# Performance work log

Hardware: AMD Instinct MI355X
Metric: run time of the kernel (lower is better)

## Reference

```python
import jax, jax.numpy as jnp
import numpy as np

HEADS = 8
DIM_HEAD = 64
QLEVEL = 127.0  # symmetric int8: clamp to [-128, 127]


def fake_quant(x):
    """Symmetric per-tensor int8 fake quantization with straight-through estimator."""
    delta = jnp.max(jnp.abs(x)) / QLEVEL
    xq = jnp.clip(jnp.round(x / delta), -128.0, 127.0) * delta
    return x + jax.lax.stop_gradient(xq - x)


def setup_inputs() -> dict:
    key = jax.random.key(0)
    ks = jax.random.split(key, 7)
    b, n, m, d, dc = 2, 4096, 1024, 512, 768
    return {
        "x": jax.random.normal(ks[0], (b, n, d), jnp.float32),
        "context": jax.random.normal(ks[1], (b, m, dc), jnp.float32),
        "Wq": jax.random.normal(ks[2], (d, d), jnp.float32) * 0.02,
        "Wk": jax.random.normal(ks[3], (dc, d), jnp.float32) * 0.02,
        "Wv": jax.random.normal(ks[4], (dc, d), jnp.float32) * 0.02,
        "Wo": jax.random.normal(ks[5], (d, d), jnp.float32) * 0.02,
        "bo": jnp.zeros((d,), jnp.float32),
    }


def reference(x, context, Wq, Wk, Wv, Wo, bo):
    b, n, _ = x.shape
    h, dh = HEADS, DIM_HEAD
    scale = dh ** -0.5

    q = x @ Wq            # [b, n, h*dh]
    k = context @ Wk      # [b, m, h*dh]
    v = context @ Wv      # [b, m, h*dh]

    def split(t):  # b n (h d) -> b h n d
        return t.reshape(t.shape[0], t.shape[1], h, dh).transpose(0, 2, 1, 3)

    q, k, v = split(q), split(k), split(v)

    # fake-quantize q and k before the score matmul (use_aq=True path)
    q = fake_quant(q)
    k = fake_quant(k)
    sim = jnp.einsum('bhid,bhjd->bhij', q, k) * scale  # [b, h, n, m]
    attn = jax.nn.softmax(sim, axis=-1)

    # fake-quantize attention weights and v before the AV matmul
    out = jnp.einsum('bhij,bhjd->bhid', fake_quant(attn), fake_quant(v))
    out = out.transpose(0, 2, 1, 3).reshape(b, n, h * dh)  # b h n d -> b n (h d)
    return out @ Wo + bo  # to_out[0]; to_out[-1] is Dropout (identity in eval)
```

## Files before the change

kernel.cpp:

```cpp
#include <hip/hip_runtime.h>
#include <stdint.h>

typedef float  v4f  __attribute__((ext_vector_type(4)));
typedef int    v4i  __attribute__((ext_vector_type(4)));
typedef __bf16 v8bf __attribute__((ext_vector_type(8)));
typedef __bf16 v4bf __attribute__((ext_vector_type(4)));

#define BATCH  2
#define NQ     4096
#define MK     1024
#define DMODEL 512
#define DCTX   768
#define NH     8
#define DH     64

__global__ __launch_bounds__(256) void k_prep(
    const float* __restrict__ x, const float* __restrict__ ctx,
    __bf16* __restrict__ xb, __bf16* __restrict__ cb,
    const float* __restrict__ Wq, const float* __restrict__ Wk,
    const float* __restrict__ Wv, const float* __restrict__ Wo,
    __bf16* __restrict__ Wq_t, __bf16* __restrict__ Wk_t,
    __bf16* __restrict__ Wv_t, __bf16* __restrict__ Wo_t,
    unsigned* __restrict__ scal) {
  int bx = blockIdx.x;
  if (bx < 2816) {
    const int XC = BATCH * NQ * DMODEL / 8;
    const int CC = BATCH * MK * DCTX / 8;
    int idx = bx * 256 + threadIdx.x;
    const float* src; __bf16* dst;
    if (idx < XC) { src = x + (size_t)idx * 8; dst = xb + (size_t)idx * 8; }
    else {
      int j = idx - XC;
      if (j >= CC) return;
      src = ctx + (size_t)j * 8; dst = cb + (size_t)j * 8;
    }
    float4 a = *(const float4*)src, b = *(const float4*)(src + 4);
    v8bf o = { (__bf16)a.x, (__bf16)a.y, (__bf16)a.z, (__bf16)a.w,
               (__bf16)b.x, (__bf16)b.y, (__bf16)b.z, (__bf16)b.w };
    *(v8bf*)dst = o;
    return;
  }
  int id = bx - 2816;
  if (id == 0 && threadIdx.x < 4) scal[threadIdx.x] = 0u;
  int tx = id & 15, rem = id >> 4;
  int ty = rem % 24, tz = rem / 24;
  const float* src; __bf16* dst; int K;
  switch (tz) {
    case 0:  src = Wq; dst = Wq_t; K = DMODEL; break;
    case 1:  src = Wk; dst = Wk_t; K = DCTX;   break;
    case 2:  src = Wv; dst = Wv_t; K = DCTX;   break;
    default: src = Wo; dst = Wo_t; K = DMODEL; break;
  }
  int k0 = ty * 32;
  if (k0 >= K) return;
  int n0 = tx * 32;
  __shared__ __bf16 tile[32][33];
  int c = threadIdx.x & 31, r0 = threadIdx.x >> 5;
  for (int i = 0; i < 4; ++i) {
    int r = r0 + i * 8;
    tile[c][r] = (__bf16)src[(size_t)(k0 + r) * DMODEL + n0 + c];
  }
  __syncthreads();
  for (int i = 0; i < 4; ++i) {
    int r = r0 + i * 8;
    dst[(size_t)(n0 + r) * K + k0 + c] = tile[r][c];
  }
}

template<int K_, int NC, bool BIAS, bool AMAX>
__device__ __forceinline__ void gemm_body(
    char* smemraw, const __bf16* __restrict__ A, const __bf16* __restrict__ Bt,
    float* __restrict__ C, int N, int rowBlk, int colBlk,
    const float* __restrict__ bias,
    unsigned* __restrict__ amaxLo, unsigned* __restrict__ amaxHi) {
  constexpr int CS = K_ + 8;
  constexpr int GPC = K_ / 8;
  constexpr int JT = NC / 16;
  __bf16* Bs = (__bf16*)smemraw;
  float* redmax = (float*)(smemraw + (size_t)NC * CS * 2);
  const int tid = threadIdx.x;
  const int lane = tid & 63, wave = tid >> 6;
  const int l15 = lane & 15, g = lane >> 4;
  const int col0 = colBlk * NC;
  const int row0w = rowBlk * 128 + wave * 32;

#pragma unroll
  for (int i = 0; i < NC * GPC / 256; ++i) {
    int f = i * 256 + tid;
    int c = f / GPC, w = f - c * GPC;
    *(v8bf*)(&Bs[c * CS + w * 8]) =
        *(const v8bf*)(Bt + (size_t)(col0 + c) * K_ + w * 8);
  }
  __syncthreads();

  v4f acc[2][JT] = {};
  const __bf16* a0 = A + (size_t)(row0w + l15) * K_ + g * 8;
  const __bf16* a1 = A + (size_t)(row0w + 16 + l15) * K_ + g * 8;
#pragma unroll
  for (int k0 = 0; k0 < K_; k0 += 32) {
    v8bf af0 = *(const v8bf*)(a0 + k0);
    v8bf af1 = *(const v8bf*)(a1 + k0);
#pragma unroll
    for (int j = 0; j < JT; ++j) {
      v8bf bfj = *(const v8bf*)(&Bs[(j * 16 + l15) * CS + k0 + g * 8]);
      acc[0][j] = __builtin_amdgcn_mfma_f32_16x16x32_bf16(af0, bfj, acc[0][j], 0, 0, 0);
      acc[1][j] = __builtin_amdgcn_mfma_f32_16x16x32_bf16(af1, bfj, acc[1][j], 0, 0, 0);
    }
  }

  float lmax = 0.0f;
#pragma unroll
  for (int j = 0; j < JT; ++j) {
    int col = col0 + j * 16 + l15;
    float bv = BIAS ? bias[col] : 0.0f;
#pragma unroll
    for (int i = 0; i < 2; ++i) {
#pragma unroll
      for (int r = 0; r < 4; ++r) {
        int row = row0w + i * 16 + g * 4 + r;
        float cv = acc[i][j][r] + bv;
        C[(size_t)row * N + col] = cv;
        if (AMAX) lmax = fmaxf(lmax, fabsf(cv));
      }
    }
  }
  if (AMAX) {
    for (int off = 32; off > 0; off >>= 1)
      lmax = fmaxf(lmax, __shfl_xor(lmax, off, 64));
    if (lane == 0) redmax[wave] = lmax;
    __syncthreads();
    if (tid == 0) {
      float bm = fmaxf(fmaxf(redmax[0], redmax[1]), fmaxf(redmax[2], redmax[3]));
      atomicMax(col0 < 512 ? amaxLo : amaxHi, __float_as_uint(bm));
    }
  }
}

__global__ __launch_bounds__(256, 2) void k_gemm_qkv(
    const __bf16* __restrict__ xb, const __bf16* __restrict__ Wq_t,
    float* __restrict__ qf,
    const __bf16* __restrict__ cb, const __bf16* __restrict__ Wkv_t,
    float* __restrict__ kvf, unsigned* __restrict__ scal) {
  __shared__ __align__(16) char smem[64 * (512 + 8) * 2 + 16];
  int bid = blockIdx.x;
  if (bid < 512) {
    gemm_body<512, 64, false, true>(smem, xb, Wq_t, qf, 512,
                                    bid >> 3, bid & 7, nullptr, scal + 0, scal + 0);
  } else {
    int id = bid - 512;
    gemm_body<768, 32, false, true>(smem, cb, Wkv_t, kvf, 1024,
                                    id >> 5, id & 31, nullptr, scal + 1, scal + 2);
  }
}

__global__ __launch_bounds__(256, 2) void k_gemm_out(
    const __bf16* __restrict__ o, const __bf16* __restrict__ Wo_t,
    float* __restrict__ out, const float* __restrict__ bo) {
  __shared__ __align__(16) char smem[64 * (512 + 8) * 2 + 16];
  gemm_body<512, 64, true, false>(smem, o, Wo_t, out, 512,
                                  blockIdx.x >> 3, blockIdx.x & 7, bo,
                                  nullptr, nullptr);
}

__global__ __launch_bounds__(256) void k_quant_kv(
    const float* __restrict__ kvf,
    int8_t* __restrict__ k8, int8_t* __restrict__ v8t,
    const unsigned* __restrict__ scal) {
  __shared__ int8_t tile[64][80];
  int bx = blockIdx.x;
  if (bx < 1024) {
    int j = bx * 256 + threadIdx.x;
    int r = j >> 7;
    int c4 = (j & 127) << 2;
    float4 v = *(const float4*)(kvf + (size_t)r * 1024 + c4);
    float s = 127.0f / __uint_as_float(scal[1]);
    int a0 = __float2int_rn(v.x * s), a1 = __float2int_rn(v.y * s);
    int a2 = __float2int_rn(v.z * s), a3 = __float2int_rn(v.w * s);
    a0 = max(-128, min(127, a0)); a1 = max(-128, min(127, a1));
    a2 = max(-128, min(127, a2)); a3 = max(-128, min(127, a3));
    unsigned p = (unsigned)(a0 & 255) | ((unsigned)(a1 & 255) << 8) |
                 ((unsigned)(a2 & 255) << 16) | ((unsigned)(a3 & 255) << 24);
    *(unsigned*)(k8 + (size_t)j * 4) = p;
    return;
  }
  int id = bx - 1024;
  int bh = id >> 4, b = bh >> 3, h = bh & 7;
  int j0 = (id & 15) * 64;
  const float s = 127.0f / __uint_as_float(scal[2]);
  int t = threadIdx.x;
  int j = t >> 2, dh0 = (t & 3) << 4;
  const float* src = kvf + (size_t)(b * MK + j0 + j) * 1024 + 512 + h * DH + dh0;
#pragma unroll
  for (int i = 0; i < 16; i += 4) {
    float4 v = *(const float4*)(src + i);
    int a0 = __float2int_rn(v.x * s), a1 = __float2int_rn(v.y * s);
    int a2 = __float2int_rn(v.z * s), a3 = __float2int_rn(v.w * s);
    tile[dh0 + i + 0][j] = (int8_t)max(-128, min(127, a0));
    tile[dh0 + i + 1][j] = (int8_t)max(-128, min(127, a1));
    tile[dh0 + i + 2][j] = (int8_t)max(-128, min(127, a2));
    tile[dh0 + i + 3][j] = (int8_t)max(-128, min(127, a3));
  }
  __syncthreads();
  int dh = t >> 2, jb = (t & 3) << 4;
  v4i val = *(const v4i*)(&tile[dh][jb]);
  *(v4i*)(v8t + (size_t)(bh * DH + dh) * MK + j0 + jb) = val;
}

__device__ __forceinline__ v4i quant_pack16(const float* p, float s) {
  v4i out;
#pragma unroll
  for (int q = 0; q < 4; ++q) {
    float4 v = *(const float4*)(p + q * 4);
    int a0 = __float2int_rn(v.x * s), a1 = __float2int_rn(v.y * s);
    int a2 = __float2int_rn(v.z * s), a3 = __float2int_rn(v.w * s);
    a0 = max(-128, min(127, a0)); a1 = max(-128, min(127, a1));
    a2 = max(-128, min(127, a2)); a3 = max(-128, min(127, a3));
    out[q] = (int)((unsigned)(a0 & 255) | ((unsigned)(a1 & 255) << 8) |
                   ((unsigned)(a2 & 255) << 16) | ((unsigned)(a3 & 255) << 24));
  }
  return out;
}

__global__ __launch_bounds__(256, 4) void k_pass1(
    const float* __restrict__ qf, int8_t* __restrict__ q8,
    const int8_t* __restrict__ k8,
    float* __restrict__ invz, unsigned* __restrict__ scal) {
  __shared__ __align__(16) int8_t kbuf[128 * 72];
  __shared__ float mared[4];
  int bh = blockIdx.y, b = bh >> 3, h = bh & 7;
  int wave = threadIdx.x >> 6, lane = threadIdx.x & 63;
  int l15 = lane & 15, g = lane >> 4;
  int row0 = blockIdx.x * 64;
  int myrow = row0 + wave * 16 + l15;
  const float aq = __uint_as_float(scal[0]), ak = __uint_as_float(scal[1]);
  const float alpha2 = (aq * ak) * (0.125f / (127.0f * 127.0f)) * 1.44269504f;
  const float sq = 127.0f / aq;
  const v4i z4 = {0, 0, 0, 0};
  size_t qoff = (size_t)(b * NQ + myrow) * DMODEL + h * DH + g * 16;
  v4i qfrag = quant_pack16(qf + qoff, sq);
  *(v4i*)(q8 + qoff) = qfrag;
  const int8_t* kbase = k8 + (size_t)b * MK * DMODEL + h * DH;
  const int rs = threadIdx.x >> 2, qs = (threadIdx.x & 3) * 16;

  float z[4] = {0.f, 0.f, 0.f, 0.f};
  int mi = -(1 << 30);
  for (int tile = 0; tile < 8; ++tile) {
    __syncthreads();
    *(v4i*)(&kbuf[rs * 72 + qs]) =
        *(const v4i*)(kbase + (size_t)(tile * 128 + rs) * DMODEL + qs);
    *(v4i*)(&kbuf[(rs + 64) * 72 + qs]) =
        *(const v4i*)(kbase + (size_t)(tile * 128 + rs + 64) * DMODEL + qs);
    __syncthreads();
    float zt = z[tile >> 1];
#pragma unroll
    for (int t = 0; t < 8; ++t) {
      v4i kfrag = *(const v4i*)(&kbuf[(t * 16 + l15) * 72 + g * 16]);
      v4i sa = __builtin_amdgcn_mfma_i32_16x16x64_i8(kfrag, qfrag, z4, 0, 0, 0);
      mi = max(mi, max(max(sa[0], sa[1]), max(sa[2], sa[3])));
      float e0 = __builtin_amdgcn_exp2f((float)sa[0] * alpha2);
      float e1 = __builtin_amdgcn_exp2f((float)sa[1] * alpha2);
      float e2 = __builtin_amdgcn_exp2f((float)sa[2] * alpha2);
      float e3 = __builtin_amdgcn_exp2f((float)sa[3] * alpha2);
      zt += (e0 + e1) + (e2 + e3);
    }
    z[tile >> 1] = zt;
  }
#pragma unroll
  for (int i = 0; i < 4; ++i) {
    z[i] += __shfl_xor(z[i], 16, 64);
    z[i] += __shfl_xor(z[i], 32, 64);
  }
  mi = max(mi, __shfl_xor(mi, 16, 64));
  mi = max(mi, __shfl_xor(mi, 32, 64));
  float zt = (z[0] + z[1]) + (z[2] + z[3]);
  float iz = 1.0f / zt;
  if (g == 0) invz[(size_t)bh * NQ + myrow] = iz;
  float ma = __builtin_amdgcn_exp2f((float)mi * alpha2) * iz;
#pragma unroll
  for (int off = 1; off < 16; off <<= 1)
    ma = fmaxf(ma, __shfl_xor(ma, off, 64));
  if (lane == 0) mared[wave] = ma;
  __syncthreads();
  if (threadIdx.x == 0)
    atomicMax(scal + 3,
              __float_as_uint(fmaxf(fmaxf(mared[0], mared[1]),
                                    fmaxf(mared[2], mared[3]))));
}

__global__ __launch_bounds__(256, 4) void k_pass2(
    const int8_t* __restrict__ q8, const int8_t* __restrict__ k8,
    const int8_t* __restrict__ v8t, const float* __restrict__ invz,
    const unsigned* __restrict__ scal, __bf16* __restrict__ o) {
  __shared__ __align__(16) int8_t kbuf[128 * 72];
  __shared__ __align__(16) int8_t vbuf[64 * 152];
  __shared__ __align__(16) int8_t albuf[4][16 * 152];
  int bh = blockIdx.y, b = bh >> 3, h = bh & 7;
  int wave = threadIdx.x >> 6, lane = threadIdx.x & 63;
  int l15 = lane & 15, g = lane >> 4;
  int row0 = blockIdx.x * 64;
  int myrow = row0 + wave * 16 + l15;
  const float aq = __uint_as_float(scal[0]), ak = __uint_as_float(scal[1]);
  const float avv = __uint_as_float(scal[2]), izm = __uint_as_float(scal[3]);
  const float alpha2 = (aq * ak) * (0.125f / (127.0f * 127.0f)) * 1.44269504f;
  const float oscale = (izm / 127.0f) * (avv / 127.0f);
  const float MAGIC = 12582912.0f;
  const v4i z4 = {0, 0, 0, 0};

  v4i qfrag = *(const v4i*)(q8 + (size_t)(b * NQ + myrow) * DMODEL + h * DH + g * 16);
  const float lcr = __builtin_amdgcn_logf(invz[(size_t)bh * NQ + myrow] * (127.0f / izm));
  const int8_t* kbase = k8 + (size_t)b * MK * DMODEL + h * DH;
  const int8_t* vbase = v8t + (size_t)bh * DH * MK;
  int8_t* alds = albuf[wave];
  const int rs = threadIdx.x >> 2, qs = (threadIdx.x & 3) * 16;
  const int vr = threadIdx.x >> 3, vq = (threadIdx.x & 7) * 16;

  v4i pacc[4] = {};
  for (int tile = 0; tile < 8; ++tile) {
    __syncthreads();
    *(v4i*)(&kbuf[rs * 72 + qs]) =
        *(const v4i*)(kbase + (size_t)(tile * 128 + rs) * DMODEL + qs);
    *(v4i*)(&kbuf[(rs + 64) * 72 + qs]) =
        *(const v4i*)(kbase + (size_t)(tile * 128 + rs + 64) * DMODEL + qs);
    *(v4i*)(&vbuf[vr * 152 + vq]) =
        *(const v4i*)(vbase + (size_t)vr * MK + tile * 128 + vq);
    *(v4i*)(&vbuf[(vr + 32) * 152 + vq]) =
        *(const v4i*)(vbase + (size_t)(vr + 32) * MK + tile * 128 + vq);
    __syncthreads();
#pragma unroll
    for (int t = 0; t < 8; ++t) {
      v4i kfrag = *(const v4i*)(&kbuf[(t * 16 + l15) * 72 + g * 16]);
      v4i sa = __builtin_amdgcn_mfma_i32_16x16x64_i8(kfrag, qfrag, z4, 0, 0, 0);
      float f0 = __builtin_amdgcn_exp2f(fmaf((float)sa[0], alpha2, lcr)) + MAGIC;
      float f1 = __builtin_amdgcn_exp2f(fmaf((float)sa[1], alpha2, lcr)) + MAGIC;
      float f2 = __builtin_amdgcn_exp2f(fmaf((float)sa[2], alpha2, lcr)) + MAGIC;
      float f3 = __builtin_amdgcn_exp2f(fmaf((float)sa[3], alpha2, lcr)) + MAGIC;
      unsigned packed = (__float_as_uint(f0) & 255u) |
                        ((__float_as_uint(f1) & 255u) << 8) |
                        ((__float_as_uint(f2) & 255u) << 16) |
                        (__float_as_uint(f3) << 24);
      *(unsigned*)(alds + l15 * 152 + t * 16 + g * 4) = packed;
    }
#pragma unroll
    for (int c = 0; c < 2; ++c) {
      v4i afrag = *(const v4i*)(alds + l15 * 152 + c * 64 + g * 16);
#pragma unroll
      for (int d = 0; d < 4; ++d) {
        v4i bfrag = *(const v4i*)(&vbuf[(d * 16 + l15) * 152 + c * 64 + g * 16]);
        pacc[d] = __builtin_amdgcn_mfma_i32_16x16x64_i8(afrag, bfrag, pacc[d], 0, 0, 0);
      }
    }
  }
  __bf16* obase = o + (size_t)(b * NQ + row0 + wave * 16) * DMODEL + h * DH;
#pragma unroll
  for (int d = 0; d < 4; ++d)
#pragma unroll
    for (int r = 0; r < 4; ++r)
      obase[(size_t)(g * 4 + r) * DMODEL + d * 16 + l15] =
          (__bf16)((float)pacc[d][r] * oscale);
}

extern "C" void kernel_launch(void* const* d_in, const int* in_sizes, int n_in,
                              void* d_out, int out_size, void* d_ws, size_t ws_size,
                              hipStream_t stream) {
  (void)in_sizes; (void)n_in; (void)out_size; (void)ws_size;
  const float* x   = (const float*)d_in[0];
  const float* ctx = (const float*)d_in[1];
  const float* Wq  = (const float*)d_in[2];
  const float* Wk  = (const float*)d_in[3];
  const float* Wv  = (const float*)d_in[4];
  const float* Wo  = (const float*)d_in[5];
  const float* bo  = (const float*)d_in[6];
  float* out = (float*)d_out;

  char* ws = (char*)d_ws;
  size_t off = 0;
  auto alloc = [&](size_t bytes) {
    char* p = ws + off;
    off += (bytes + 255) & ~(size_t)255;
    return p;
  };
  unsigned* scal = (unsigned*)alloc(16);
  __bf16* Wq_t = (__bf16*)alloc((size_t)512 * 512 * 2);
  __bf16* Wk_t = (__bf16*)alloc((size_t)512 * 768 * 2);
  __bf16* Wv_t = (__bf16*)alloc((size_t)512 * 768 * 2);
  __bf16* Wo_t = (__bf16*)alloc((size_t)512 * 512 * 2);
  __bf16* xb   = (__bf16*)alloc((size_t)BATCH * NQ * DMODEL * 2);
  __bf16* cb   = (__bf16*)alloc((size_t)BATCH * MK * DCTX * 2);
  float* qf  = (float*)alloc((size_t)BATCH * NQ * DMODEL * 4);
  float* kvf = (float*)alloc((size_t)BATCH * MK * 1024 * 4);
  int8_t* q8 = (int8_t*)alloc((size_t)BATCH * NQ * DMODEL);
  int8_t* k8 = (int8_t*)alloc((size_t)BATCH * MK * DMODEL);
  int8_t* v8t = (int8_t*)alloc((size_t)BATCH * NH * DH * MK);
  float* invz = (float*)alloc((size_t)BATCH * NH * NQ * 4);
  __bf16* o = (__bf16*)qf;

  k_prep<<<4352, 256, 0, stream>>>(x, ctx, xb, cb, Wq, Wk, Wv, Wo,
                                   Wq_t, Wk_t, Wv_t, Wo_t, scal);
  k_gemm_qkv<<<1024, 256, 0, stream>>>(xb, Wq_t, qf, cb, Wk_t, kvf, scal);
  k_quant_kv<<<1280, 256, 0, stream>>>(kvf, k8, v8t, scal);
  k_pass1<<<dim3(64, 16), 256, 0, stream>>>(qf, q8, k8, invz, scal);
  k_pass2<<<dim3(64, 16), 256, 0, stream>>>(q8, k8, v8t, invz, scal, o);
  k_gemm_out<<<512, 256, 0, stream>>>(o, Wo_t, out, bo);
}
```

Before: 183.3 us.

## Fuse fp32-to-bf16 input conversion into QKV GEMM and prefetch K/V tiles

Drops the separate x/context bf16 conversion pass and converts fp32 activations to bf16 inside the QKV GEMM A-operand load. This removes a full write and reread of the converted inputs. The attention passes now prefetch the next K/V tile into registers while computing on the current one. Pass2 also swaps the MFMA operand order so each lane writes four contiguous bf16 outputs as one vector store. In exchange, the GEMM reads twice as many bytes per A load and keeps more registers live for the prefetch.

```diff
diff --git a/kernel.cpp b/kernel.cpp
--- a/kernel.cpp
+++ b/kernel.cpp
@@ -15,32 +15,12 @@
 #define DH     64
 
 __global__ __launch_bounds__(256) void k_prep(
-    const float* __restrict__ x, const float* __restrict__ ctx,
-    __bf16* __restrict__ xb, __bf16* __restrict__ cb,
     const float* __restrict__ Wq, const float* __restrict__ Wk,
     const float* __restrict__ Wv, const float* __restrict__ Wo,
     __bf16* __restrict__ Wq_t, __bf16* __restrict__ Wk_t,
     __bf16* __restrict__ Wv_t, __bf16* __restrict__ Wo_t,
     unsigned* __restrict__ scal) {
-  int bx = blockIdx.x;
-  if (bx < 2816) {
-    const int XC = BATCH * NQ * DMODEL / 8;
-    const int CC = BATCH * MK * DCTX / 8;
-    int idx = bx * 256 + threadIdx.x;
-    const float* src; __bf16* dst;
-    if (idx < XC) { src = x + (size_t)idx * 8; dst = xb + (size_t)idx * 8; }
-    else {
-      int j = idx - XC;
-      if (j >= CC) return;
-      src = ctx + (size_t)j * 8; dst = cb + (size_t)j * 8;
-    }
-    float4 a = *(const float4*)src, b = *(const float4*)(src + 4);
-    v8bf o = { (__bf16)a.x, (__bf16)a.y, (__bf16)a.z, (__bf16)a.w,
-               (__bf16)b.x, (__bf16)b.y, (__bf16)b.z, (__bf16)b.w };
-    *(v8bf*)dst = o;
-    return;
-  }
-  int id = bx - 2816;
+  int id = blockIdx.x;
   if (id == 0 && threadIdx.x < 4) scal[threadIdx.x] = 0u;
   int tx = id & 15, rem = id >> 4;
   int ty = rem % 24, tz = rem / 24;
@@ -67,9 +47,19 @@
   }
 }
 
-template<int K_, int NC, bool BIAS, bool AMAX>
+__device__ __forceinline__ v8bf load_a8(const __bf16* p) {
+  return *(const v8bf*)p;
+}
+__device__ __forceinline__ v8bf load_a8(const float* p) {
+  float4 a = *(const float4*)p, b = *(const float4*)(p + 4);
+  v8bf o = { (__bf16)a.x, (__bf16)a.y, (__bf16)a.z, (__bf16)a.w,
+             (__bf16)b.x, (__bf16)b.y, (__bf16)b.z, (__bf16)b.w };
+  return o;
+}
+
+template<int K_, int NC, bool BIAS, bool AMAX, typename AT>
 __device__ __forceinline__ void gemm_body(
-    char* smemraw, const __bf16* __restrict__ A, const __bf16* __restrict__ Bt,
+    char* smemraw, const AT* __restrict__ A, const __bf16* __restrict__ Bt,
     float* __restrict__ C, int N, int rowBlk, int colBlk,
     const float* __restrict__ bias,
     unsigned* __restrict__ amaxLo, unsigned* __restrict__ amaxHi) {
@@ -94,12 +84,12 @@
   __syncthreads();
 
   v4f acc[2][JT] = {};
-  const __bf16* a0 = A + (size_t)(row0w + l15) * K_ + g * 8;
-  const __bf16* a1 = A + (size_t)(row0w + 16 + l15) * K_ + g * 8;
+  const AT* a0 = A + (size_t)(row0w + l15) * K_ + g * 8;
+  const AT* a1 = A + (size_t)(row0w + 16 + l15) * K_ + g * 8;
 #pragma unroll
   for (int k0 = 0; k0 < K_; k0 += 32) {
-    v8bf af0 = *(const v8bf*)(a0 + k0);
-    v8bf af1 = *(const v8bf*)(a1 + k0);
+    v8bf af0 = load_a8(a0 + k0);
+    v8bf af1 = load_a8(a1 + k0);
 #pragma unroll
     for (int j = 0; j < JT; ++j) {
       v8bf bfj = *(const v8bf*)(&Bs[(j * 16 + l15) * CS + k0 + g * 8]);
@@ -137,19 +127,21 @@
 }
 
 __global__ __launch_bounds__(256, 2) void k_gemm_qkv(
-    const __bf16* __restrict__ xb, const __bf16* __restrict__ Wq_t,
+    const float* __restrict__ x, const __bf16* __restrict__ Wq_t,
     float* __restrict__ qf,
-    const __bf16* __restrict__ cb, const __bf16* __restrict__ Wkv_t,
+    const float* __restrict__ ctx, const __bf16* __restrict__ Wkv_t,
     float* __restrict__ kvf, unsigned* __restrict__ scal) {
   __shared__ __align__(16) char smem[64 * (512 + 8) * 2 + 16];
   int bid = blockIdx.x;
   if (bid < 512) {
-    gemm_body<512, 64, false, true>(smem, xb, Wq_t, qf, 512,
-                                    bid >> 3, bid & 7, nullptr, scal + 0, scal + 0);
+    gemm_body<512, 64, false, true, float>(smem, x, Wq_t, qf, 512,
+                                           bid >> 3, bid & 7, nullptr,
+                                           scal + 0, scal + 0);
   } else {
     int id = bid - 512;
-    gemm_body<768, 32, false, true>(smem, cb, Wkv_t, kvf, 1024,
-                                    id >> 5, id & 31, nullptr, scal + 1, scal + 2);
+    gemm_body<768, 32, false, true, float>(smem, ctx, Wkv_t, kvf, 1024,
+                                           id >> 5, id & 31, nullptr,
+                                           scal + 1, scal + 2);
   }
 }
 
@@ -157,9 +149,9 @@
     const __bf16* __restrict__ o, const __bf16* __restrict__ Wo_t,
     float* __restrict__ out, const float* __restrict__ bo) {
   __shared__ __align__(16) char smem[64 * (512 + 8) * 2 + 16];
-  gemm_body<512, 64, true, false>(smem, o, Wo_t, out, 512,
-                                  blockIdx.x >> 3, blockIdx.x & 7, bo,
-                                  nullptr, nullptr);
+  gemm_body<512, 64, true, false, __bf16>(smem, o, Wo_t, out, 512,
+                                          blockIdx.x >> 3, blockIdx.x & 7, bo,
+                                          nullptr, nullptr);
 }
 
 __global__ __launch_bounds__(256) void k_quant_kv(
@@ -241,16 +233,22 @@
   *(v4i*)(q8 + qoff) = qfrag;
   const int8_t* kbase = k8 + (size_t)b * MK * DMODEL + h * DH;
   const int rs = threadIdx.x >> 2, qs = (threadIdx.x & 3) * 16;
+  const int8_t* kls = kbase + (size_t)rs * DMODEL + qs;
+
+  v4i kp0 = *(const v4i*)(kls);
+  v4i kp1 = *(const v4i*)(kls + (size_t)64 * DMODEL);
 
   float z[4] = {0.f, 0.f, 0.f, 0.f};
   int mi = -(1 << 30);
   for (int tile = 0; tile < 8; ++tile) {
     __syncthreads();
-    *(v4i*)(&kbuf[rs * 72 + qs]) =
-        *(const v4i*)(kbase + (size_t)(tile * 128 + rs) * DMODEL + qs);
-    *(v4i*)(&kbuf[(rs + 64) * 72 + qs]) =
-        *(const v4i*)(kbase + (size_t)(tile * 128 + rs + 64) * DMODEL + qs);
+    *(v4i*)(&kbuf[rs * 72 + qs]) = kp0;
+    *(v4i*)(&kbuf[(rs + 64) * 72 + qs]) = kp1;
     __syncthreads();
+    if (tile < 7) {
+      kp0 = *(const v4i*)(kls + (size_t)((tile + 1) * 128) * DMODEL);
+      kp1 = *(const v4i*)(kls + (size_t)((tile + 1) * 128 + 64) * DMODEL);
+    }
     float zt = z[tile >> 1];
 #pragma unroll
     for (int t = 0; t < 8; ++t) {
@@ -313,19 +311,28 @@
   int8_t* alds = albuf[wave];
   const int rs = threadIdx.x >> 2, qs = (threadIdx.x & 3) * 16;
   const int vr = threadIdx.x >> 3, vq = (threadIdx.x & 7) * 16;
+  const int8_t* kls = kbase + (size_t)rs * DMODEL + qs;
+  const int8_t* vls = vbase + (size_t)vr * MK + vq;
+
+  v4i kp0 = *(const v4i*)(kls);
+  v4i kp1 = *(const v4i*)(kls + (size_t)64 * DMODEL);
+  v4i vp0 = *(const v4i*)(vls);
+  v4i vp1 = *(const v4i*)(vls + (size_t)32 * MK);
 
   v4i pacc[4] = {};
   for (int tile = 0; tile < 8; ++tile) {
     __syncthreads();
-    *(v4i*)(&kbuf[rs * 72 + qs]) =
-        *(const v4i*)(kbase + (size_t)(tile * 128 + rs) * DMODEL + qs);
-    *(v4i*)(&kbuf[(rs + 64) * 72 + qs]) =
-        *(const v4i*)(kbase + (size_t)(tile * 128 + rs + 64) * DMODEL + qs);
-    *(v4i*)(&vbuf[vr * 152 + vq]) =
-        *(const v4i*)(vbase + (size_t)vr * MK + tile * 128 + vq);
-    *(v4i*)(&vbuf[(vr + 32) * 152 + vq]) =
-        *(const v4i*)(vbase + (size_t)(vr + 32) * MK + tile * 128 + vq);
+    *(v4i*)(&kbuf[rs * 72 + qs]) = kp0;
+    *(v4i*)(&kbuf[(rs + 64) * 72 + qs]) = kp1;
+    *(v4i*)(&vbuf[vr * 152 + vq]) = vp0;
+    *(v4i*)(&vbuf[(vr + 32) * 152 + vq]) = vp1;
     __syncthreads();
+    if (tile < 7) {
+      kp0 = *(const v4i*)(kls + (size_t)((tile + 1) * 128) * DMODEL);
+      kp1 = *(const v4i*)(kls + (size_t)((tile + 1) * 128 + 64) * DMODEL);
+      vp0 = *(const v4i*)(vls + (tile + 1) * 128);
+      vp1 = *(const v4i*)(vls + (size_t)32 * MK + (tile + 1) * 128);
+    }
 #pragma unroll
     for (int t = 0; t < 8; ++t) {
       v4i kfrag = *(const v4i*)(&kbuf[(t * 16 + l15) * 72 + g * 16]);
@@ -345,18 +352,20 @@
       v4i afrag = *(const v4i*)(alds + l15 * 152 + c * 64 + g * 16);
 #pragma unroll
       for (int d = 0; d < 4; ++d) {
-        v4i bfrag = *(const v4i*)(&vbuf[(d * 16 + l15) * 152 + c * 64 + g * 16]);
-        pacc[d] = __builtin_amdgcn_mfma_i32_16x16x64_i8(afrag, bfrag, pacc[d], 0, 0, 0);
+        v4i vfrag = *(const v4i*)(&vbuf[(d * 16 + l15) * 152 + c * 64 + g * 16]);
+        pacc[d] = __builtin_amdgcn_mfma_i32_16x16x64_i8(vfrag, afrag, pacc[d], 0, 0, 0);
       }
     }
   }
-  __bf16* obase = o + (size_t)(b * NQ + row0 + wave * 16) * DMODEL + h * DH;
-#pragma unroll
-  for (int d = 0; d < 4; ++d)
+  __bf16* obase = o + (size_t)(b * NQ + row0 + wave * 16 + l15) * DMODEL + h * DH;
+#pragma unroll
+  for (int d = 0; d < 4; ++d) {
+    v4bf ov;
 #pragma unroll
     for (int r = 0; r < 4; ++r)
-      obase[(size_t)(g * 4 + r) * DMODEL + d * 16 + l15] =
-          (__bf16)((float)pacc[d][r] * oscale);
+      ov[r] = (__bf16)((float)pacc[d][r] * oscale);
+    *(v4bf*)(obase + d * 16 + g * 4) = ov;
+  }
 }
 
 extern "C" void kernel_launch(void* const* d_in, const int* in_sizes, int n_in,
@@ -384,8 +393,6 @@
   __bf16* Wk_t = (__bf16*)alloc((size_t)512 * 768 * 2);
   __bf16* Wv_t = (__bf16*)alloc((size_t)512 * 768 * 2);
   __bf16* Wo_t = (__bf16*)alloc((size_t)512 * 512 * 2);
-  __bf16* xb   = (__bf16*)alloc((size_t)BATCH * NQ * DMODEL * 2);
-  __bf16* cb   = (__bf16*)alloc((size_t)BATCH * MK * DCTX * 2);
   float* qf  = (float*)alloc((size_t)BATCH * NQ * DMODEL * 4);
   float* kvf = (float*)alloc((size_t)BATCH * MK * 1024 * 4);
   int8_t* q8 = (int8_t*)alloc((size_t)BATCH * NQ * DMODEL);
@@ -394,9 +401,9 @@
   float* invz = (float*)alloc((size_t)BATCH * NH * NQ * 4);
   __bf16* o = (__bf16*)qf;
 
-  k_prep<<<4352, 256, 0, stream>>>(x, ctx, xb, cb, Wq, Wk, Wv, Wo,
+  k_prep<<<1536, 256, 0, stream>>>(Wq, Wk, Wv, Wo,
                                    Wq_t, Wk_t, Wv_t, Wo_t, scal);
-  k_gemm_qkv<<<1024, 256, 0, stream>>>(xb, Wq_t, qf, cb, Wk_t, kvf, scal);
+  k_gemm_qkv<<<1024, 256, 0, stream>>>(x, Wq_t, qf, ctx, Wk_t, kvf, scal);
   k_quant_kv<<<1280, 256, 0, stream>>>(kvf, k8, v8t, scal);
   k_pass1<<<dim3(64, 16), 256, 0, stream>>>(qf, q8, k8, invz, scal);
   k_pass2<<<dim3(64, 16), 256, 0, stream>>>(q8, k8, v8t, invz, scal, o);
```

After: 193.8 us. 5.7% more time.
